# Optimization experiments

Hardware: AMD Instinct MI355X
Metric: run time of the kernel (lower is better)

Reference implementation:

```python
import jax, jax.numpy as jnp
import numpy as np

B, LQ, LV = 32, 64, 128
QS, FS, BN = 512, 1024, 512

def setup_inputs() -> dict:
    key = jax.random.key(0)
    k1, k2, k3, k4, k5 = jax.random.split(key, 5)
    s = lambda n: 1.0 / np.sqrt(n)
    return {
        "phr_feats": jax.random.normal(k1, (B, LQ, QS), dtype=jnp.float32),
        "vis_feats": jax.random.normal(k2, (B, LV, FS), dtype=jnp.float32),
        "W": jax.random.uniform(k3, (BN, QS), jnp.float32, -s(QS), s(QS)),
        "U": jax.random.uniform(k4, (BN, FS), jnp.float32, -s(FS), s(FS)),
        "b": jnp.ones((BN,), dtype=jnp.float32),
        "w": jax.random.uniform(k5, (1, BN), jnp.float32, -s(BN), s(BN)),
    }

def reference(phr_feats, vis_feats, W, U, b, w):
    # Wh: [B,Lq,BN], Uv: [B,Lv,BN]
    Wh = jnp.einsum('bqd,nd->bqn', phr_feats, W)
    Uv = jnp.einsum('bvf,nf->bvn', vis_feats, U)
    # broadcast add + tanh: [B,Lq,Lv,BN]
    t = jnp.tanh(Wh[:, :, None, :] + Uv[:, None, :, :] + b)
    energies = jnp.einsum('bqvn,n->bqv', t, w[0])  # squeeze(-1)
    weights = jax.nn.softmax(energies, axis=2)
    aligned = jnp.einsum('bqv,bvf->bqf', weights, vis_feats)
    semantic_group_feats = jnp.concatenate([phr_feats, aligned], axis=2)
    return (semantic_group_feats, weights, energies)
```

## Files before the change

### kernel.cpp

```cpp
#include <hip/hip_runtime.h>

#define NB  32
#define NLQ 64
#define NLV 128
#define NQS 512
#define NFS 1024
#define NBN 512
#define CC  2.8853900817779268f

typedef float  floatx4 __attribute__((ext_vector_type(4)));
typedef __bf16 bf16x8  __attribute__((ext_vector_type(8)));
typedef unsigned short us;

__device__ __forceinline__ us f2bf(float f) {
    unsigned int u = __float_as_uint(f);
    u += 0x7fffu + ((u >> 16) & 1u);
    return (us)(u >> 16);
}
__device__ __forceinline__ unsigned int pktrunc(float lo, float hi) {
    return __builtin_amdgcn_perm(__float_as_uint(hi), __float_as_uint(lo), 0x07060302u);
}
__device__ __forceinline__ float blo(unsigned int u) {
    return __uint_as_float(u << 16);
}
__device__ __forceinline__ float bhi(unsigned int u) {
    return __uint_as_float(u & 0xffff0000u);
}

__device__ __forceinline__ void gemm64(
    us* As, us* Bs,
    const float* __restrict__ A, const float* __restrict__ Bt,
    const float* __restrict__ bias, us* __restrict__ C,
    int K, int bx, int by, int hasb,
    float* __restrict__ sgf, us* __restrict__ visb)
{
    const int tid  = threadIdx.x;
    const int m0   = bx * 64;
    const int n0   = by * 64;
    const int wave = tid >> 6;
    const int lane = tid & 63;
    const int wm   = (wave >> 1) * 32;
    const int wn   = (wave & 1) * 32;
    const int srow = tid >> 2;
    const int sk   = (tid & 3) * 8;
    const int fm   = lane & 15;
    const int fko  = (lane >> 4) * 8;

    floatx4 acc[2][2] = {};
    const float* ag = A  + (size_t)(m0 + srow) * K + sk;
    const float* bg = Bt + (size_t)(n0 + srow) * K + sk;

    float4 a0 = *(const float4*)(ag),     a1 = *(const float4*)(ag + 4);
    float4 b0 = *(const float4*)(bg),     b1 = *(const float4*)(bg + 4);

    for (int k0 = 0; k0 < K; k0 += 32) {
        __syncthreads();
        if (sgf) {
            float* d = sgf + (size_t)(m0 + srow) * (NQS + NFS) + k0 + sk;
            *(float4*)d       = a0;
            *(float4*)(d + 4) = a1;
        }
        uint4 av = { pktrunc(a0.x, a0.y), pktrunc(a0.z, a0.w),
                     pktrunc(a1.x, a1.y), pktrunc(a1.z, a1.w) };
        uint4 bv = { pktrunc(b0.x, b0.y), pktrunc(b0.z, b0.w),
                     pktrunc(b1.x, b1.y), pktrunc(b1.z, b1.w) };
        if (visb)
            *(uint4*)(visb + (size_t)(m0 + srow) * NFS + k0 + sk) = av;
        *(uint4*)(As + srow * 40 + sk) = av;
        *(uint4*)(Bs + srow * 40 + sk) = bv;
        const int kn = k0 + 32;
        if (kn < K) {
            a0 = *(const float4*)(ag + kn); a1 = *(const float4*)(ag + kn + 4);
            b0 = *(const float4*)(bg + kn); b1 = *(const float4*)(bg + kn + 4);
        }
        __syncthreads();
        bf16x8 am[2], bn[2];
        #pragma unroll
        for (int i = 0; i < 2; ++i)
            am[i] = *(const bf16x8*)(As + (wm + 16 * i + fm) * 40 + fko);
        #pragma unroll
        for (int j = 0; j < 2; ++j)
            bn[j] = *(const bf16x8*)(Bs + (wn + 16 * j + fm) * 40 + fko);
        #pragma unroll
        for (int i = 0; i < 2; ++i)
            #pragma unroll
            for (int j = 0; j < 2; ++j)
                acc[i][j] = __builtin_amdgcn_mfma_f32_16x16x32_bf16(am[i], bn[j], acc[i][j], 0, 0, 0);
    }

    const int cr = (lane >> 4) * 4;
    const int cc = lane & 15;
    #pragma unroll
    for (int i = 0; i < 2; ++i)
        #pragma unroll
        for (int j = 0; j < 2; ++j)
            #pragma unroll
            for (int r = 0; r < 4; ++r) {
                int gm = m0 + wm + 16 * i + cr + r;
                int gn = n0 + wn + 16 * j + cc;
                float v = acc[i][j][r];
                if (hasb) v += bias[gn];
                C[(size_t)gm * NBN + gn] = f2bf(__builtin_amdgcn_exp2f(CC * v));
            }
}

__global__ __launch_bounds__(256) void gemm_both(
    const float* __restrict__ phr, const float* __restrict__ W,
    const float* __restrict__ bias,
    const float* __restrict__ vis, const float* __restrict__ U,
    us* __restrict__ whY, us* __restrict__ uvY,
    float* __restrict__ out_sgf, us* __restrict__ vis_b)
{
    __shared__ __align__(16) us As[64 * 40];
    __shared__ __align__(16) us Bs[64 * 40];
    int blk = blockIdx.x;
    if (blk < 256) {
        int bx = blk % 32, by = blk / 32;
        gemm64(As, Bs, phr, W, bias, whY, NQS, bx, by, 1,
               by == 0 ? out_sgf : nullptr, nullptr);
    } else {
        blk -= 256;
        int bx = blk % 64, by = blk / 64;
        gemm64(As, Bs, vis, U, bias, uvY, NFS, bx, by, 0,
               nullptr, by == 0 ? vis_b : nullptr);
    }
}

__global__ __launch_bounds__(512, 4) void attn_fused(
    const us* __restrict__ whY,
    const us* __restrict__ uvY,
    const float* __restrict__ wvec,
    const us* __restrict__ vis_b,
    float* __restrict__ out_sgf, float* __restrict__ out_w, float* __restrict__ out_e)
{
    const float LOG2E = 1.4426950408889634f;
    const int blk  = blockIdx.x;
    const int b    = blk & 31;
    const int qg   = blk >> 5;
    const int tid  = threadIdx.x;
    const int wave = tid >> 6;
    const int lane = tid & 63;

    __shared__ float e_s[4][128];
    __shared__ float p_s[4][128];

    const int n0 = lane << 3;
    float Yq[4][8];
    #pragma unroll
    for (int qq = 0; qq < 4; ++qq) {
        uint4 y = *(const uint4*)(whY + (size_t)(b * NLQ + qg * 4 + qq) * NBN + n0);
        Yq[qq][0] = blo(y.x); Yq[qq][1] = bhi(y.x);
        Yq[qq][2] = blo(y.y); Yq[qq][3] = bhi(y.y);
        Yq[qq][4] = blo(y.z); Yq[qq][5] = bhi(y.z);
        Yq[qq][6] = blo(y.w); Yq[qq][7] = bhi(y.w);
    }
    float4 w0 = *(const float4*)(wvec + n0);
    float4 w1 = *(const float4*)(wvec + n0 + 4);
    float nw2[8] = { 2.f*w0.x, 2.f*w0.y, 2.f*w0.z, 2.f*w0.w,
                     2.f*w1.x, 2.f*w1.y, 2.f*w1.z, 2.f*w1.w };
    float sumw = w0.x + w0.y + w0.z + w0.w + w1.x + w1.y + w1.z + w1.w;
    #pragma unroll
    for (int off = 32; off; off >>= 1) sumw += __shfl_xor(sumw, off);

    #pragma unroll
    for (int vblk = 0; vblk < 2; ++vblk) {
        const us* base = uvY + ((size_t)b * NLV + wave * 16 + vblk * 8) * NBN + n0;
        float s[4][8];
        #pragma unroll
        for (int j = 0; j < 8; ++j) {
            uint4 u = *(const uint4*)(base + (size_t)j * NBN);
            float yv[8] = { blo(u.x), bhi(u.x), blo(u.y), bhi(u.y),
                            blo(u.z), bhi(u.z), blo(u.w), bhi(u.w) };
            #pragma unroll
            for (int qq = 0; qq < 4; ++qq) {
                float a = 0.f;
                #pragma unroll
                for (int k = 0; k < 8; ++k) {
                    float d = fmaf(yv[k], Yq[qq][k], 1.f);
                    a = fmaf(nw2[k], __builtin_amdgcn_rcpf(d), a);
                }
                s[qq][j] = a;
            }
        }
        #pragma unroll
        for (int qq = 0; qq < 4; ++qq) {
            #pragma unroll
            for (int m = 8; m <= 32; m <<= 1)
                #pragma unroll
                for (int j = 0; j < 8; ++j) s[qq][j] += __shfl_xor(s[qq][j], m);
            float t[4];
            #pragma unroll
            for (int p = 0; p < 4; ++p) {
                float ae = s[qq][2*p]     + __shfl_xor(s[qq][2*p],     1);
                float bo = s[qq][2*p + 1] + __shfl_xor(s[qq][2*p + 1], 1);
                t[p] = (lane & 1) ? bo : ae;
            }
            float u2[2];
            #pragma unroll
            for (int p = 0; p < 2; ++p) {
                float ae = t[2*p]     + __shfl_xor(t[2*p],     2);
                float bo = t[2*p + 1] + __shfl_xor(t[2*p + 1], 2);
                u2[p] = (lane & 2) ? bo : ae;
            }
            float ae = u2[0] + __shfl_xor(u2[0], 4);
            float bo = u2[1] + __shfl_xor(u2[1], 4);
            float r  = (lane & 4) ? bo : ae;
            if (lane < 8) e_s[qq][wave * 16 + vblk * 8 + lane] = sumw - r;
        }
    }
    __syncthreads();

    if (wave < 4) {
        const int q = wave;
        float e0 = e_s[q][lane];
        float e1 = e_s[q][lane + 64];
        float m = fmaxf(e0, e1);
        #pragma unroll
        for (int off = 32; off; off >>= 1) m = fmaxf(m, __shfl_xor(m, off));
        float x0 = __builtin_amdgcn_exp2f((e0 - m) * LOG2E);
        float x1 = __builtin_amdgcn_exp2f((e1 - m) * LOG2E);
        float ss = x0 + x1;
        #pragma unroll
        for (int off = 32; off; off >>= 1) ss += __shfl_xor(ss, off);
        float inv = __builtin_amdgcn_rcpf(ss);
        float p0 = x0 * inv, p1 = x1 * inv;
        size_t o = (size_t)(b * NLQ + qg * 4 + q) * NLV;
        out_w[o + lane]      = p0;
        out_w[o + lane + 64] = p1;
        out_e[o + lane]      = e0;
        out_e[o + lane + 64] = e1;
        p_s[q][lane]      = p0;
        p_s[q][lane + 64] = p1;
    }
    __syncthreads();

    const int f0 = tid << 1;
    float2 acc[4] = {};
    const us* vb = vis_b + (size_t)b * NLV * NFS + f0;
    for (int v0 = 0; v0 < NLV; v0 += 4) {
        float4 pv[4];
        #pragma unroll
        for (int qq = 0; qq < 4; ++qq) pv[qq] = *(const float4*)&p_s[qq][v0];
        #pragma unroll
        for (int dv = 0; dv < 4; ++dv) {
            unsigned int u = *(const unsigned int*)(vb + (size_t)(v0 + dv) * NFS);
            float x0 = blo(u), x1 = bhi(u);
            #pragma unroll
            for (int qq = 0; qq < 4; ++qq) {
                float p = (dv == 0) ? pv[qq].x : (dv == 1) ? pv[qq].y
                        : (dv == 2) ? pv[qq].z : pv[qq].w;
                acc[qq].x = fmaf(p, x0, acc[qq].x);
                acc[qq].y = fmaf(p, x1, acc[qq].y);
            }
        }
    }
    #pragma unroll
    for (int qq = 0; qq < 4; ++qq) {
        size_t row = (size_t)(b * NLQ + qg * 4 + qq);
        *(float2*)(out_sgf + row * (NQS + NFS) + NQS + f0) = acc[qq];
    }
}

extern "C" void kernel_launch(void* const* d_in, const int* in_sizes, int n_in,
                              void* d_out, int out_size, void* d_ws, size_t ws_size,
                              hipStream_t stream) {
    const float* phr  = (const float*)d_in[0];
    const float* vis  = (const float*)d_in[1];
    const float* W    = (const float*)d_in[2];
    const float* U    = (const float*)d_in[3];
    const float* bias = (const float*)d_in[4];
    const float* wvec = (const float*)d_in[5];

    char* ws = (char*)d_ws;
    us* whY   = (us*)ws;
    us* uvY   = (us*)(ws + (2u << 20));
    us* vis_b = (us*)(ws + (6u << 20));

    float* out     = (float*)d_out;
    float* out_sgf = out;
    float* out_w   = out_sgf + (size_t)NB * NLQ * (NQS + NFS);
    float* out_e   = out_w   + (size_t)NB * NLQ * NLV;

    gemm_both<<<768, 256, 0, stream>>>(phr, W, bias, vis, U, whY, uvY,
                                       out_sgf, vis_b);
    attn_fused<<<NB * 16, 512, 0, stream>>>(whY, uvY, wvec, vis_b,
                                            out_sgf, out_w, out_e);
}
```

Before: 140.8 us.

## Split attention into energy/softmax kernel and MFMA aligned-features kernel with transposed layouts

```diff
diff --git a/kernel.cpp b/kernel.cpp
--- a/kernel.cpp
+++ b/kernel.cpp
@@ -30,9 +30,10 @@
 __device__ __forceinline__ void gemm64(
     us* As, us* Bs,
     const float* __restrict__ A, const float* __restrict__ Bt,
-    const float* __restrict__ bias, us* __restrict__ C,
-    int K, int bx, int by, int hasb,
-    float* __restrict__ sgf, us* __restrict__ visb)
+    const float* __restrict__ bias,
+    float* __restrict__ whYp, us* __restrict__ uvYTp,
+    int K, int bx, int by,
+    float* __restrict__ sgf, us* __restrict__ visbT)
 {
     const int tid  = threadIdx.x;
     const int m0   = bx * 64;
@@ -64,8 +65,6 @@
                      pktrunc(a1.x, a1.y), pktrunc(a1.z, a1.w) };
         uint4 bv = { pktrunc(b0.x, b0.y), pktrunc(b0.z, b0.w),
                      pktrunc(b1.x, b1.y), pktrunc(b1.z, b1.w) };
-        if (visb)
-            *(uint4*)(visb + (size_t)(m0 + srow) * NFS + k0 + sk) = av;
         *(uint4*)(As + srow * 40 + sk) = av;
         *(uint4*)(Bs + srow * 40 + sk) = bv;
         const int kn = k0 + 32;
@@ -86,179 +85,224 @@
             #pragma unroll
             for (int j = 0; j < 2; ++j)
                 acc[i][j] = __builtin_amdgcn_mfma_f32_16x16x32_bf16(am[i], bn[j], acc[i][j], 0, 0, 0);
+
+        if (visbT) {
+            const int bb = m0 >> 7, vbase = m0 & 127;
+            #pragma unroll
+            for (int h = 0; h < 2; ++h) {
+                int idx = h * 256 + tid;
+                int f   = idx >> 4;
+                int v0  = (idx & 15) * 4;
+                us e0 = As[(v0 + 0) * 40 + f];
+                us e1 = As[(v0 + 1) * 40 + f];
+                us e2 = As[(v0 + 2) * 40 + f];
+                us e3 = As[(v0 + 3) * 40 + f];
+                uint2 pk2 = { (unsigned int)e0 | ((unsigned int)e1 << 16),
+                              (unsigned int)e2 | ((unsigned int)e3 << 16) };
+                *(uint2*)(visbT + ((size_t)bb * NFS + k0 + f) * NLV + vbase + v0) = pk2;
+            }
+        }
     }
 
     const int cr = (lane >> 4) * 4;
     const int cc = lane & 15;
-    #pragma unroll
-    for (int i = 0; i < 2; ++i)
-        #pragma unroll
-        for (int j = 0; j < 2; ++j)
-            #pragma unroll
-            for (int r = 0; r < 4; ++r) {
-                int gm = m0 + wm + 16 * i + cr + r;
-                int gn = n0 + wn + 16 * j + cc;
-                float v = acc[i][j][r];
-                if (hasb) v += bias[gn];
-                C[(size_t)gm * NBN + gn] = f2bf(__builtin_amdgcn_exp2f(CC * v));
-            }
+    if (whYp) {
+        #pragma unroll
+        for (int i = 0; i < 2; ++i)
+            #pragma unroll
+            for (int j = 0; j < 2; ++j)
+                #pragma unroll
+                for (int r = 0; r < 4; ++r) {
+                    int gm = m0 + wm + 16 * i + cr + r;
+                    int gn = n0 + wn + 16 * j + cc;
+                    float v = acc[i][j][r] + bias[gn];
+                    whYp[(size_t)gm * NBN + gn] = __builtin_amdgcn_exp2f(CC * v);
+                }
+    } else {
+        #pragma unroll
+        for (int i = 0; i < 2; ++i)
+            #pragma unroll
+            for (int j = 0; j < 2; ++j) {
+                int gm0 = m0 + wm + 16 * i + cr;
+                int gn  = n0 + wn + 16 * j + cc;
+                int bb  = gm0 >> 7, v = gm0 & 127;
+                unsigned int y0 = f2bf(__builtin_amdgcn_exp2f(CC * acc[i][j][0]));
+                unsigned int y1 = f2bf(__builtin_amdgcn_exp2f(CC * acc[i][j][1]));
+                unsigned int y2 = f2bf(__builtin_amdgcn_exp2f(CC * acc[i][j][2]));
+                unsigned int y3 = f2bf(__builtin_amdgcn_exp2f(CC * acc[i][j][3]));
+                uint2 pk2 = { y0 | (y1 << 16), y2 | (y3 << 16) };
+                *(uint2*)(uvYTp + ((size_t)bb * NBN + gn) * NLV + v) = pk2;
+            }
+    }
 }
 
 __global__ __launch_bounds__(256) void gemm_both(
     const float* __restrict__ phr, const float* __restrict__ W,
     const float* __restrict__ bias,
     const float* __restrict__ vis, const float* __restrict__ U,
-    us* __restrict__ whY, us* __restrict__ uvY,
-    float* __restrict__ out_sgf, us* __restrict__ vis_b)
+    float* __restrict__ whY, us* __restrict__ uvYT,
+    float* __restrict__ out_sgf, us* __restrict__ visbT)
 {
     __shared__ __align__(16) us As[64 * 40];
     __shared__ __align__(16) us Bs[64 * 40];
     int blk = blockIdx.x;
     if (blk < 256) {
         int bx = blk % 32, by = blk / 32;
-        gemm64(As, Bs, phr, W, bias, whY, NQS, bx, by, 1,
+        gemm64(As, Bs, phr, W, bias, whY, nullptr, NQS, bx, by,
                by == 0 ? out_sgf : nullptr, nullptr);
     } else {
         blk -= 256;
         int bx = blk % 64, by = blk / 64;
-        gemm64(As, Bs, vis, U, bias, uvY, NFS, bx, by, 0,
-               nullptr, by == 0 ? vis_b : nullptr);
-    }
-}
-
-__global__ __launch_bounds__(512, 4) void attn_fused(
-    const us* __restrict__ whY,
-    const us* __restrict__ uvY,
+        gemm64(As, Bs, vis, U, bias, nullptr, uvYT, NFS, bx, by,
+               nullptr, by == 0 ? visbT : nullptr);
+    }
+}
+
+__global__ __launch_bounds__(256) void energize(
+    const float* __restrict__ whY,
+    const us* __restrict__ uvYT,
     const float* __restrict__ wvec,
-    const us* __restrict__ vis_b,
-    float* __restrict__ out_sgf, float* __restrict__ out_w, float* __restrict__ out_e)
+    float* __restrict__ out_w, float* __restrict__ out_e,
+    us* __restrict__ p_bf, us* __restrict__ p_lo)
 {
     const float LOG2E = 1.4426950408889634f;
-    const int blk  = blockIdx.x;
-    const int b    = blk & 31;
-    const int qg   = blk >> 5;
+    int blk = blockIdx.x;
+    blk = (blk & 7) * 64 + (blk >> 3);
+    const int b    = blk >> 4;
+    const int qq4  = blk & 15;
+    const int tid  = threadIdx.x;
+    const int wave = __builtin_amdgcn_readfirstlane(tid >> 6);
+    const int lane = tid & 63;
+    const int q0   = qq4 * 4;
+
+    __shared__ float part[4][4][NLV];
+
+    float4 sw0 = *(const float4*)(wvec + lane * 8);
+    float4 sw1 = *(const float4*)(wvec + lane * 8 + 4);
+    float sumw = sw0.x + sw0.y + sw0.z + sw0.w + sw1.x + sw1.y + sw1.z + sw1.w;
+    #pragma unroll
+    for (int off = 32; off; off >>= 1) sumw += __shfl_xor(sumw, off);
+
+    const float* yqp = whY + (size_t)(b * NLQ + q0) * NBN + wave * 128;
+    const float* wp  = wvec + wave * 128;
+    const us*    uvp = uvYT + ((size_t)b * NBN + wave * 128) * NLV + 2 * lane;
+
+    float acc[4][2] = {};
+    #pragma unroll 2
+    for (int nc = 0; nc < 128; nc += 8) {
+        unsigned int yv[8];
+        #pragma unroll
+        for (int k = 0; k < 8; ++k)
+            yv[k] = *(const unsigned int*)(uvp + (size_t)(nc + k) * NLV);
+        #pragma unroll
+        for (int k = 0; k < 8; ++k) {
+            float x0 = blo(yv[k]), x1 = bhi(yv[k]);
+            float wk = wp[nc + k];
+            #pragma unroll
+            for (int q = 0; q < 4; ++q) {
+                float yq = yqp[q * NBN + nc + k];
+                float d0 = fmaf(x0, yq, 1.f);
+                float d1 = fmaf(x1, yq, 1.f);
+                acc[q][0] = fmaf(wk, __builtin_amdgcn_rcpf(d0), acc[q][0]);
+                acc[q][1] = fmaf(wk, __builtin_amdgcn_rcpf(d1), acc[q][1]);
+            }
+        }
+    }
+    #pragma unroll
+    for (int q = 0; q < 4; ++q) {
+        float2 t = { acc[q][0], acc[q][1] };
+        *(float2*)&part[q][wave][2 * lane] = t;
+    }
+    __syncthreads();
+
+    const int q = wave;
+    float s0 = 0.f, s1 = 0.f;
+    #pragma unroll
+    for (int nq = 0; nq < 4; ++nq) {
+        s0 += part[q][nq][2 * lane];
+        s1 += part[q][nq][2 * lane + 1];
+    }
+    float e0 = sumw - 2.f * s0;
+    float e1 = sumw - 2.f * s1;
+    float m = fmaxf(e0, e1);
+    #pragma unroll
+    for (int off = 32; off; off >>= 1) m = fmaxf(m, __shfl_xor(m, off));
+    float x0 = __builtin_amdgcn_exp2f((e0 - m) * LOG2E);
+    float x1 = __builtin_amdgcn_exp2f((e1 - m) * LOG2E);
+    float ss = x0 + x1;
+    #pragma unroll
+    for (int off = 32; off; off >>= 1) ss += __shfl_xor(ss, off);
+    float inv = __builtin_amdgcn_rcpf(ss);
+    float p0 = x0 * inv, p1 = x1 * inv;
+
+    const size_t row = (size_t)(b * NLQ + q0 + q);
+    float2 ep = { e0, e1 };
+    float2 pp = { p0, p1 };
+    *(float2*)(out_e + row * NLV + 2 * lane) = ep;
+    *(float2*)(out_w + row * NLV + 2 * lane) = pp;
+    unsigned int pb0 = f2bf(p0), pb1 = f2bf(p1);
+    float lo0 = p0 - __uint_as_float(pb0 << 16);
+    float lo1 = p1 - __uint_as_float(pb1 << 16);
+    unsigned int lb0 = f2bf(lo0), lb1 = f2bf(lo1);
+    *(unsigned int*)(p_bf + row * NLV + 2 * lane) = pb0 | (pb1 << 16);
+    *(unsigned int*)(p_lo + row * NLV + 2 * lane) = lb0 | (lb1 << 16);
+}
+
+__global__ __launch_bounds__(256) void aligned_mfma(
+    const us* __restrict__ p_bf, const us* __restrict__ p_lo,
+    const us* __restrict__ visbT,
+    float* __restrict__ out_sgf)
+{
+    int blk = blockIdx.x;
+    blk = (blk & 7) * 64 + (blk >> 3);
+    const int b    = blk >> 4;
+    const int ft   = blk & 15;
     const int tid  = threadIdx.x;
     const int wave = tid >> 6;
     const int lane = tid & 63;
-
-    __shared__ float e_s[4][128];
-    __shared__ float p_s[4][128];
-
-    const int n0 = lane << 3;
-    float Yq[4][8];
-    #pragma unroll
-    for (int qq = 0; qq < 4; ++qq) {
-        uint4 y = *(const uint4*)(whY + (size_t)(b * NLQ + qg * 4 + qq) * NBN + n0);
-        Yq[qq][0] = blo(y.x); Yq[qq][1] = bhi(y.x);
-        Yq[qq][2] = blo(y.y); Yq[qq][3] = bhi(y.y);
-        Yq[qq][4] = blo(y.z); Yq[qq][5] = bhi(y.z);
-        Yq[qq][6] = blo(y.w); Yq[qq][7] = bhi(y.w);
-    }
-    float4 w0 = *(const float4*)(wvec + n0);
-    float4 w1 = *(const float4*)(wvec + n0 + 4);
-    float nw2[8] = { 2.f*w0.x, 2.f*w0.y, 2.f*w0.z, 2.f*w0.w,
-                     2.f*w1.x, 2.f*w1.y, 2.f*w1.z, 2.f*w1.w };
-    float sumw = w0.x + w0.y + w0.z + w0.w + w1.x + w1.y + w1.z + w1.w;
-    #pragma unroll
-    for (int off = 32; off; off >>= 1) sumw += __shfl_xor(sumw, off);
-
-    #pragma unroll
-    for (int vblk = 0; vblk < 2; ++vblk) {
-        const us* base = uvY + ((size_t)b * NLV + wave * 16 + vblk * 8) * NBN + n0;
-        float s[4][8];
-        #pragma unroll
-        for (int j = 0; j < 8; ++j) {
-            uint4 u = *(const uint4*)(base + (size_t)j * NBN);
-            float yv[8] = { blo(u.x), bhi(u.x), blo(u.y), bhi(u.y),
-                            blo(u.z), bhi(u.z), blo(u.w), bhi(u.w) };
-            #pragma unroll
-            for (int qq = 0; qq < 4; ++qq) {
-                float a = 0.f;
-                #pragma unroll
-                for (int k = 0; k < 8; ++k) {
-                    float d = fmaf(yv[k], Yq[qq][k], 1.f);
-                    a = fmaf(nw2[k], __builtin_amdgcn_rcpf(d), a);
-                }
-                s[qq][j] = a;
-            }
-        }
-        #pragma unroll
-        for (int qq = 0; qq < 4; ++qq) {
-            #pragma unroll
-            for (int m = 8; m <= 32; m <<= 1)
-                #pragma unroll
-                for (int j = 0; j < 8; ++j) s[qq][j] += __shfl_xor(s[qq][j], m);
-            float t[4];
-            #pragma unroll
-            for (int p = 0; p < 4; ++p) {
-                float ae = s[qq][2*p]     + __shfl_xor(s[qq][2*p],     1);
-                float bo = s[qq][2*p + 1] + __shfl_xor(s[qq][2*p + 1], 1);
-                t[p] = (lane & 1) ? bo : ae;
-            }
-            float u2[2];
-            #pragma unroll
-            for (int p = 0; p < 2; ++p) {
-                float ae = t[2*p]     + __shfl_xor(t[2*p],     2);
-                float bo = t[2*p + 1] + __shfl_xor(t[2*p + 1], 2);
-                u2[p] = (lane & 2) ? bo : ae;
-            }
-            float ae = u2[0] + __shfl_xor(u2[0], 4);
-            float bo = u2[1] + __shfl_xor(u2[1], 4);
-            float r  = (lane & 4) ? bo : ae;
-            if (lane < 8) e_s[qq][wave * 16 + vblk * 8 + lane] = sumw - r;
-        }
-    }
-    __syncthreads();
-
-    if (wave < 4) {
-        const int q = wave;
-        float e0 = e_s[q][lane];
-        float e1 = e_s[q][lane + 64];
-        float m = fmaxf(e0, e1);
-        #pragma unroll
-        for (int off = 32; off; off >>= 1) m = fmaxf(m, __shfl_xor(m, off));
-        float x0 = __builtin_amdgcn_exp2f((e0 - m) * LOG2E);
-        float x1 = __builtin_amdgcn_exp2f((e1 - m) * LOG2E);
-        float ss = x0 + x1;
-        #pragma unroll
-        for (int off = 32; off; off >>= 1) ss += __shfl_xor(ss, off);
-        float inv = __builtin_amdgcn_rcpf(ss);
-        float p0 = x0 * inv, p1 = x1 * inv;
-        size_t o = (size_t)(b * NLQ + qg * 4 + q) * NLV;
-        out_w[o + lane]      = p0;
-        out_w[o + lane + 64] = p1;
-        out_e[o + lane]      = e0;
-        out_e[o + lane + 64] = e1;
-        p_s[q][lane]      = p0;
-        p_s[q][lane + 64] = p1;
-    }
-    __syncthreads();
-
-    const int f0 = tid << 1;
-    float2 acc[4] = {};
-    const us* vb = vis_b + (size_t)b * NLV * NFS + f0;
-    for (int v0 = 0; v0 < NLV; v0 += 4) {
-        float4 pv[4];
-        #pragma unroll
-        for (int qq = 0; qq < 4; ++qq) pv[qq] = *(const float4*)&p_s[qq][v0];
-        #pragma unroll
-        for (int dv = 0; dv < 4; ++dv) {
-            unsigned int u = *(const unsigned int*)(vb + (size_t)(v0 + dv) * NFS);
-            float x0 = blo(u), x1 = bhi(u);
-            #pragma unroll
-            for (int qq = 0; qq < 4; ++qq) {
-                float p = (dv == 0) ? pv[qq].x : (dv == 1) ? pv[qq].y
-                        : (dv == 2) ? pv[qq].z : pv[qq].w;
-                acc[qq].x = fmaf(p, x0, acc[qq].x);
-                acc[qq].y = fmaf(p, x1, acc[qq].y);
-            }
-        }
-    }
-    #pragma unroll
-    for (int qq = 0; qq < 4; ++qq) {
-        size_t row = (size_t)(b * NLQ + qg * 4 + qq);
-        *(float2*)(out_sgf + row * (NQS + NFS) + NQS + f0) = acc[qq];
-    }
+    const int wm   = (wave >> 1) * 32;
+    const int wf   = (wave & 1) * 32;
+    const int fm   = lane & 15;
+    const int fko  = (lane >> 4) * 8;
+
+    floatx4 acc[2][2] = {};
+    const us* pA  = p_bf + ((size_t)b * NLQ + wm + fm) * NLV + fko;
+    const us* pAl = p_lo + ((size_t)b * NLQ + wm + fm) * NLV + fko;
+    const us* pB  = visbT + ((size_t)b * NFS + ft * 64 + wf + fm) * NLV + fko;
+
+    #pragma unroll
+    for (int ks = 0; ks < 4; ++ks) {
+        bf16x8 a[2], al[2], bb[2];
+        #pragma unroll
+        for (int i = 0; i < 2; ++i) {
+            a[i]  = *(const bf16x8*)(pA  + (size_t)i * 16 * NLV + ks * 32);
+            al[i] = *(const bf16x8*)(pAl + (size_t)i * 16 * NLV + ks * 32);
+        }
+        #pragma unroll
+        for (int j = 0; j < 2; ++j)
+            bb[j] = *(const bf16x8*)(pB + (size_t)j * 16 * NLV + ks * 32);
+        #pragma unroll
+        for (int i = 0; i < 2; ++i)
+            #pragma unroll
+            for (int j = 0; j < 2; ++j) {
+                acc[i][j] = __builtin_amdgcn_mfma_f32_16x16x32_bf16(a[i],  bb[j], acc[i][j], 0, 0, 0);
+                acc[i][j] = __builtin_amdgcn_mfma_f32_16x16x32_bf16(al[i], bb[j], acc[i][j], 0, 0, 0);
+            }
+    }
+
+    const int cr = (lane >> 4) * 4;
+    const int cc = lane & 15;
+    #pragma unroll
+    for (int i = 0; i < 2; ++i)
+        #pragma unroll
+        for (int j = 0; j < 2; ++j)
+            #pragma unroll
+            for (int r = 0; r < 4; ++r) {
+                int q = wm + 16 * i + cr + r;
+                int f = ft * 64 + wf + 16 * j + cc;
+                size_t row = (size_t)b * NLQ + q;
+                out_sgf[row * (NQS + NFS) + NQS + f] = acc[i][j][r];
+            }
 }
 
 extern "C" void kernel_launch(void* const* d_in, const int* in_sizes, int n_in,
@@ -272,17 +316,19 @@
     const float* wvec = (const float*)d_in[5];
 
     char* ws = (char*)d_ws;
-    us* whY   = (us*)ws;
-    us* uvY   = (us*)(ws + (2u << 20));
-    us* vis_b = (us*)(ws + (6u << 20));
+    float* whY  = (float*)ws;
+    us* uvYT    = (us*)(ws + (4u << 20));
+    us* visbT   = (us*)(ws + (8u << 20));
+    us* p_bf    = (us*)(ws + (16u << 20));
+    us* p_lo    = (us*)(ws + (16u << 20) + (512u << 10));
 
     float* out     = (float*)d_out;
     float* out_sgf = out;
     float* out_w   = out_sgf + (size_t)NB * NLQ * (NQS + NFS);
     float* out_e   = out_w   + (size_t)NB * NLQ * NLV;
 
-    gemm_both<<<768, 256, 0, stream>>>(phr, W, bias, vis, U, whY, uvY,
-                                       out_sgf, vis_b);
-    attn_fused<<<NB * 16, 512, 0, stream>>>(whY, uvY, wvec, vis_b,
-                                            out_sgf, out_w, out_e);
-}
+    gemm_both<<<768, 256, 0, stream>>>(phr, W, bias, vis, U,
+                                       whY, uvYT, out_sgf, visbT);
+    energize<<<512, 256, 0, stream>>>(whY, uvYT, wvec, out_w, out_e, p_bf, p_lo);
+    aligned_mfma<<<512, 256, 0, stream>>>(p_bf, p_lo, visbT, out_sgf);
+}
```

New measurement: 128.2 us. -9.0%, faster.
